# Kernel optimization log

Hardware: AMD Instinct MI355X
Metric: run time of the kernel (lower is better)

## Reference

```python
import jax, jax.numpy as jnp
import numpy as np

BN_EPS = 1e-5


def setup_inputs() -> dict:
    key = jax.random.key(0)
    ks = jax.random.split(key, 5)
    B, C, T, V = 64, 64, 300, 25
    O, N = 128, 8  # out_channels, num_adj
    x = jax.random.normal(ks[0], (B, C, T, V), dtype=jnp.float32)
    # adjacency: row-normalized so powers A^1..A^8 stay well-conditioned
    A = jax.random.uniform(ks[1], (V, V), dtype=jnp.float32)
    A = A / jnp.sum(A, axis=1, keepdims=True)
    W = jax.random.normal(ks[2], (N, O // N, C), dtype=jnp.float32) * 0.05  # per-branch 1x1 conv weights
    Wr = jax.random.normal(ks[3], (O, C), dtype=jnp.float32) * 0.05          # residual 1x1 conv weight
    br = jnp.zeros((O,), dtype=jnp.float32)                                   # residual conv bias
    gamma = jnp.ones((O,), dtype=jnp.float32)
    beta = jnp.zeros((O,), dtype=jnp.float32)
    return {"x": x, "A": A, "W": W, "Wr": Wr, "br": br, "gamma": gamma, "beta": beta}


def reference(x, A, W, Wr, br, gamma, beta):
    # x: [B, C, T, V]; A: [V, V]; W: [num_adj, O//num_adj, C]
    num_adj = W.shape[0]
    outs = []
    A_pow = A  # A_list[i] = A^(i+1), matching _split_adjacency_matrix
    for i in range(num_adj):
        g = jnp.einsum('bcfj,jk->bcfk', x, A_pow)           # graph conv on joints
        outs.append(jnp.einsum('oc,bcfk->bofk', W[i], g))   # 1x1 conv (no bias)
        A_pow = A_pow @ A
    out = jnp.concatenate(outs, axis=1)                      # [B, O, T, V]
    residual = jnp.einsum('oc,bcfj->bofj', Wr, x) + br[None, :, None, None]
    out = out + residual
    # BatchNorm2d (training-mode batch statistics over B, T, V per channel)
    mean = jnp.mean(out, axis=(0, 2, 3), keepdims=True)
    var = jnp.var(out, axis=(0, 2, 3), keepdims=True)
    out = gamma[None, :, None, None] * (out - mean) / jnp.sqrt(var + BN_EPS) + beta[None, :, None, None]
    return jax.nn.relu(out)
```

## Files before the change

### kernel.cpp

```cpp
#include <hip/hip_runtime.h>
#include <hip/hip_bf16.h>

#define B_  64
#define C_  64
#define T_  300
#define V_  25
#define O_  128
#define TV  (T_*V_)
#define BTV (B_*T_*V_)
#define HS_STRIDE 258
#define HS_ROWS 57
#define NPF 9600

typedef __bf16 bf16x8 __attribute__((ext_vector_type(8)));
typedef float f32x4 __attribute__((ext_vector_type(4)));

#define WSB_AF    0ull
#define WSB_WT    18432ull
#define WSB_PSC   51200ull
#define WSB_PSQ   4966400ull
#define WSB_SCL   9881600ull
#define WSB_SFT   9882112ull
#define WSB_Y     9882624ull
#define WS_NEED2  132762624ull

static __device__ __forceinline__ unsigned short f2bf(float f) {
    unsigned int u = __float_as_uint(f);
    unsigned int r = (u + 0x7fffu + ((u >> 16) & 1u)) >> 16;
    return (unsigned short)r;
}
static __device__ __forceinline__ float bf2f(unsigned short u) {
    return __uint_as_float(((unsigned int)u) << 16);
}

__global__ __launch_bounds__(256) void k_prep(const float* __restrict__ A,
                                              const float* __restrict__ W,
                                              const float* __restrict__ Wr,
                                              unsigned short* __restrict__ AF,
                                              unsigned short* __restrict__ Wt) {
    const int tid = threadIdx.x;
    if (blockIdx.x == 0) {
        __shared__ float Pall[8][625];
        for (int p = tid; p < 625; p += 256) Pall[0][p] = A[p];
        __syncthreads();
        for (int i = 1; i < 8; i++) {
            for (int p = tid; p < 625; p += 256) {
                int r = p / 25, c = p - r * 25;
                float s = 0.f;
                #pragma unroll 5
                for (int j = 0; j < 25; j++) s = fmaf(Pall[i-1][r*25 + j], A[j*25 + c], s);
                Pall[i][p] = s;
            }
            __syncthreads();
        }
        for (int idx = tid; idx < 18 * 64; idx += 256) {
            int fi = idx >> 6, l = idx & 63, qq = l >> 4, tt = l & 15;
            unsigned short v[8];
            #pragma unroll
            for (int e = 0; e < 8; e++) {
                int j = qq * 8 + e;
                float val = 0.f;
                if (fi < 16) {
                    int i = fi >> 1, k = (fi & 1) * 16 + tt;
                    if (j < 25 && k < 25) val = Pall[i][j * 25 + k];
                } else {
                    int k = (fi - 16) * 16 + tt;
                    if (j < 25 && k < 25 && j == k) val = 1.f;
                }
                v[e] = f2bf(val);
            }
            *(uint4*)(AF + idx * 8) = *(uint4*)v;
        }
    } else {
        const int oc = tid;
        const float* src = (oc < 128) ? (W + oc * 64) : (Wr + (oc - 128) * 64);
        unsigned short row[64];
        #pragma unroll
        for (int c = 0; c < 64; c++) row[c] = f2bf(src[c]);
        #pragma unroll
        for (int cc = 0; cc < 8; cc++)
            *(uint4*)(Wt + oc * 64 + cc * 8) = *(uint4*)(row + cc * 8);
    }
}

__global__ __launch_bounds__(256, 4) void k_fuse(const float* __restrict__ x,
                                                 const unsigned short* __restrict__ Wt,
                                                 const unsigned short* __restrict__ AF,
                                                 unsigned short* __restrict__ Yg,
                                                 float* __restrict__ psc,
                                                 float* __restrict__ psq) {
    __shared__ __align__(16) unsigned short SM[4096 + HS_ROWS * HS_STRIDE];
    unsigned short* As = SM;
    unsigned short* Hs = SM + 4096;
    const int tg = blockIdx.x, b = blockIdx.y;
    const int tid = threadIdx.x, wv = tid >> 6, ln = tid & 63;
    const int q = ln >> 4, t = ln & 15;

    for (int p = tid; p < 1600; p += 256) {
        int c = p / 25, e = p - c * 25;
        float2 f = *(const float2*)(x + ((size_t)(b * 64 + c)) * TV + tg * 50 + e * 2);
        int r0 = e * 2;
        As[r0 * 64 + (((c >> 3) ^ (r0 & 7)) << 3) + (c & 7)]         = f2bf(f.x);
        As[(r0+1) * 64 + (((c >> 3) ^ ((r0+1) & 7)) << 3) + (c & 7)] = f2bf(f.y);
    }
    for (int w = tid; w < 448; w += 256) ((unsigned int*)As)[1600 + w] = 0u;
    for (int w = tid; w < 903; w += 256) ((unsigned int*)Hs)[6450 + w] = 0u;
    __syncthreads();

    {
        const int oq = wv;
        f32x4 acc[4][4] = {};
        #pragma unroll
        for (int ks = 0; ks < 2; ks++) {
            const unsigned short* wb = Wt + (oq * 64 + t) * 64 + q * 8 + ks * 32;
            bf16x8 bv[4], af[4];
            #pragma unroll
            for (int ni = 0; ni < 4; ni++) bv[ni] = *(const bf16x8*)(wb + ni * 1024);
            #pragma unroll
            for (int mi = 0; mi < 4; mi++) {
                int row = mi * 16 + t;
                af[mi] = *(const bf16x8*)(As + row * 64 + (((ks * 4 + q) ^ (row & 7)) << 3));
            }
            #pragma unroll
            for (int mi = 0; mi < 4; mi++)
                #pragma unroll
                for (int ni = 0; ni < 4; ni++)
                    acc[mi][ni] = __builtin_amdgcn_mfma_f32_16x16x32_bf16(bv[ni], af[mi], acc[mi][ni], 0, 0, 0);
        }
        #pragma unroll
        for (int mi = 0; mi < 4; mi++) {
            int row = mi * 16 + t;
            if (row < 50) {
                #pragma unroll
                for (int ni = 0; ni < 4; ni++) {
                    int co = oq * 64 + ni * 16 + q * 4;
                    unsigned int* dst = (unsigned int*)(Hs + row * HS_STRIDE + co);
                    dst[0] = (unsigned int)f2bf(acc[mi][ni][0]) | ((unsigned int)f2bf(acc[mi][ni][1]) << 16);
                    dst[1] = (unsigned int)f2bf(acc[mi][ni][2]) | ((unsigned int)f2bf(acc[mi][ni][3]) << 16);
                }
            }
        }
    }
    __syncthreads();

    const int s = wv >> 1, bh = wv & 1;
    const bf16x8* AFp = (const bf16x8*)AF;
    const bf16x8 id0 = AFp[16 * 64 + ln];
    const bf16x8 id1 = AFp[17 * 64 + ln];
    f32x4 acc2[4][2];
    #pragma unroll
    for (int ii = 0; ii < 4; ii++) { acc2[ii][0] = (f32x4){0,0,0,0}; acc2[ii][1] = (f32x4){0,0,0,0}; }
    const int rowq = (s * 25 + q * 8) * HS_STRIDE + t;
    #pragma unroll
    for (int ii = 0; ii < 4; ii++) {
        const int i = bh * 4 + ii;
        unsigned short hm[8], hr[8];
        #pragma unroll
        for (int e = 0; e < 8; e++) {
            int a = rowq + e * HS_STRIDE + i * 16;
            hm[e] = Hs[a];
            hr[e] = Hs[a + 128];
        }
        bf16x8 bm = *(bf16x8*)hm;
        bf16x8 brs = *(bf16x8*)hr;
        bf16x8 a0 = AFp[(i * 2 + 0) * 64 + ln];
        bf16x8 a1 = AFp[(i * 2 + 1) * 64 + ln];
        acc2[ii][0] = __builtin_amdgcn_mfma_f32_16x16x32_bf16(id0, brs, acc2[ii][0], 0, 0, 0);
        acc2[ii][1] = __builtin_amdgcn_mfma_f32_16x16x32_bf16(id1, brs, acc2[ii][1], 0, 0, 0);
        acc2[ii][0] = __builtin_amdgcn_mfma_f32_16x16x32_bf16(a0, bm, acc2[ii][0], 0, 0, 0);
        acc2[ii][1] = __builtin_amdgcn_mfma_f32_16x16x32_bf16(a1, bm, acc2[ii][1], 0, 0, 0);
    }
    float* ps = (float*)SM;
    float* qs = ps + 256;
    #pragma unroll
    for (int ii = 0; ii < 4; ii++) {
        float si = 0.f, qi = 0.f;
        #pragma unroll
        for (int mt = 0; mt < 2; mt++)
            #pragma unroll
            for (int r = 0; r < 4; r++) {
                float v = acc2[ii][mt][r];
                si += v; qi += v * v;
            }
        si += __shfl_xor(si, 16); si += __shfl_xor(si, 32);
        qi += __shfl_xor(qi, 16); qi += __shfl_xor(qi, 32);
        if (ln < 16) {
            ps[s * 128 + (bh * 4 + ii) * 16 + t] = si;
            qs[s * 128 + (bh * 4 + ii) * 16 + t] = qi;
        }
    }
    #pragma unroll
    for (int ii = 0; ii < 4; ii++)
        #pragma unroll
        for (int mt = 0; mt < 2; mt++)
            #pragma unroll
            for (int r = 0; r < 4; r++) {
                int k = mt * 16 + q * 4 + r;
                if (k < 25)
                    Hs[(s * 25 + k) * HS_STRIDE + (bh * 4 + ii) * 16 + t] = f2bf(acc2[ii][mt][r]);
            }
    __syncthreads();
    if (tid < 128) {
        float S = ps[tid] + ps[128 + tid];
        float Q = qs[tid] + qs[128 + tid];
        int blk = b * 150 + tg;
        psc[(size_t)blk * 128 + tid] = S;
        psq[(size_t)blk * 128 + tid] = Q;
    }
    for (int idx = tid; idx < 3200; idx += 256) {
        int o = idx / 25, w = idx - o * 25;
        unsigned int d = (unsigned int)Hs[(w * 2) * HS_STRIDE + o]
                       | ((unsigned int)Hs[(w * 2 + 1) * HS_STRIDE + o] << 16);
        *(unsigned int*)(Yg + (size_t)(b * 128 + o) * TV + tg * 50 + w * 2) = d;
    }
}

__global__ __launch_bounds__(256) void k_fin2(const float* __restrict__ psc,
                                              const float* __restrict__ psq,
                                              const float* __restrict__ gamma,
                                              const float* __restrict__ beta,
                                              float* __restrict__ scale,
                                              float* __restrict__ shift) {
    const int o = blockIdx.x, tid = threadIdx.x;
    float S = 0.f, Q = 0.f;
    for (int i = tid; i < NPF; i += 256) {
        S += psc[(size_t)i * 128 + o];
        Q += psq[(size_t)i * 128 + o];
    }
    #pragma unroll
    for (int m = 1; m < 64; m <<= 1) { S += __shfl_xor(S, m); Q += __shfl_xor(Q, m); }
    __shared__ float ls[4], lq[4];
    int w = tid >> 6;
    if ((tid & 63) == 0) { ls[w] = S; lq[w] = Q; }
    __syncthreads();
    if (tid == 0) {
        float St = ls[0] + ls[1] + ls[2] + ls[3];
        float Qt = lq[0] + lq[1] + lq[2] + lq[3];
        float inv = 1.f / (float)BTV;
        float mean = St * inv;
        float var = Qt * inv - mean * mean;
        float sc = gamma[o] / sqrtf(var + 1e-5f);
        scale[o] = sc;
        shift[o] = beta[o] - mean * sc;
    }
}

__global__ __launch_bounds__(256) void k_norm2(const unsigned short* __restrict__ Y,
                                               const float* __restrict__ scale,
                                               const float* __restrict__ shift,
                                               float* __restrict__ out) {
    size_t e0 = ((size_t)blockIdx.x * 256 + threadIdx.x) * 8;
    #pragma unroll
    for (int g = 0; g < 2; g++) {
        size_t e = e0 + (size_t)g * 4;
        int o = (int)((e / 7500) & 127);
        float sc = scale[o], sh = shift[o];
        uint2 v = *(const uint2*)(Y + e);
        float4 d;
        d.x = fmaxf(fmaf(bf2f((unsigned short)(v.x & 0xffffu)), sc, sh), 0.f);
        d.y = fmaxf(fmaf(bf2f((unsigned short)(v.x >> 16)),     sc, sh), 0.f);
        d.z = fmaxf(fmaf(bf2f((unsigned short)(v.y & 0xffffu)), sc, sh), 0.f);
        d.w = fmaxf(fmaf(bf2f((unsigned short)(v.y >> 16)),     sc, sh), 0.f);
        *(float4*)(out + e) = d;
    }
}

extern "C" void kernel_launch(void* const* d_in, const int* in_sizes, int n_in,
                              void* d_out, int out_size, void* d_ws, size_t ws_size,
                              hipStream_t stream) {
    const float* x     = (const float*)d_in[0];
    const float* A     = (const float*)d_in[1];
    const float* W     = (const float*)d_in[2];
    const float* Wr    = (const float*)d_in[3];
    const float* gamma = (const float*)d_in[5];
    const float* beta  = (const float*)d_in[6];
    float* out = (float*)d_out;
    char* wsb  = (char*)d_ws;
    if (ws_size < (size_t)WS_NEED2) return;

    unsigned short* AF  = (unsigned short*)(wsb + WSB_AF);
    unsigned short* Wt  = (unsigned short*)(wsb + WSB_WT);
    float*          psc = (float*)(wsb + WSB_PSC);
    float*          psq = (float*)(wsb + WSB_PSQ);
    float*          scl = (float*)(wsb + WSB_SCL);
    float*          sft = (float*)(wsb + WSB_SFT);
    unsigned short* Y   = (unsigned short*)(wsb + WSB_Y);

    k_prep<<<2, 256, 0, stream>>>(A, W, Wr, AF, Wt);
    k_fuse<<<dim3(150, 64), 256, 0, stream>>>(x, Wt, AF, Y, psc, psq);
    k_fin2<<<128, 256, 0, stream>>>(psc, psq, gamma, beta, scl, sft);
    k_norm2<<<30000, 256, 0, stream>>>(Y, scl, sft, out);
}
```

Before: 267.7 us.

## Double block tile to 4 time steps and transpose intermediate LDS layout with XOR swizzle

```diff
diff --git a/kernel.cpp b/kernel.cpp
--- a/kernel.cpp
+++ b/kernel.cpp
@@ -8,9 +8,7 @@
 #define O_  128
 #define TV  (T_*V_)
 #define BTV (B_*T_*V_)
-#define HS_STRIDE 258
-#define HS_ROWS 57
-#define NPF 9600
+#define NPF 4800
 
 typedef __bf16 bf16x8 __attribute__((ext_vector_type(8)));
 typedef float f32x4 __attribute__((ext_vector_type(4)));
@@ -83,32 +81,39 @@
     }
 }
 
-__global__ __launch_bounds__(256, 4) void k_fuse(const float* __restrict__ x,
+__global__ __launch_bounds__(512, 2) void k_fuse(const float* __restrict__ x,
                                                  const unsigned short* __restrict__ Wt,
                                                  const unsigned short* __restrict__ AF,
                                                  unsigned short* __restrict__ Yg,
                                                  float* __restrict__ psc,
                                                  float* __restrict__ psq) {
-    __shared__ __align__(16) unsigned short SM[4096 + HS_ROWS * HS_STRIDE];
-    unsigned short* As = SM;
-    unsigned short* Hs = SM + 4096;
+    __shared__ __align__(16) unsigned short SM[8192 + 256 * 128];
+    unsigned short* As  = SM;
+    unsigned short* Hs2 = SM + 8192;
     const int tg = blockIdx.x, b = blockIdx.y;
     const int tid = threadIdx.x, wv = tid >> 6, ln = tid & 63;
     const int q = ln >> 4, t = ln & 15;
 
-    for (int p = tid; p < 1600; p += 256) {
-        int c = p / 25, e = p - c * 25;
-        float2 f = *(const float2*)(x + ((size_t)(b * 64 + c)) * TV + tg * 50 + e * 2);
-        int r0 = e * 2;
-        As[r0 * 64 + (((c >> 3) ^ (r0 & 7)) << 3) + (c & 7)]         = f2bf(f.x);
-        As[(r0+1) * 64 + (((c >> 3) ^ ((r0+1) & 7)) << 3) + (c & 7)] = f2bf(f.y);
-    }
-    for (int w = tid; w < 448; w += 256) ((unsigned int*)As)[1600 + w] = 0u;
-    for (int w = tid; w < 903; w += 256) ((unsigned int*)Hs)[6450 + w] = 0u;
+    for (int p = tid; p < 1600; p += 512) {
+        int c = p / 25, e4 = p - c * 25;
+        float4 f = *(const float4*)(x + ((size_t)(b * 64 + c)) * TV + tg * 100 + e4 * 4);
+        float vv[4] = { f.x, f.y, f.z, f.w };
+        #pragma unroll
+        for (int u = 0; u < 4; u++) {
+            int r = e4 * 4 + u;
+            As[r * 64 + (((c >> 3) ^ (r & 7)) << 3) + (c & 7)] = f2bf(vv[u]);
+        }
+    }
+    for (int w = tid; w < 896; w += 512) ((unsigned int*)As)[3200 + w] = 0u;
+    for (int gi = tid; gi < 1024; gi += 512) {
+        int oc = gi >> 2, s = gi & 3;
+        int g = (s * 4 + 3) ^ (oc & 15);
+        *(uint4*)(Hs2 + oc * 128 + g * 8) = (uint4){0u, 0u, 0u, 0u};
+    }
     __syncthreads();
 
     {
-        const int oq = wv;
+        const int rb = wv >> 2, oq = wv & 3;
         f32x4 acc[4][4] = {};
         #pragma unroll
         for (int ks = 0; ks < 2; ks++) {
@@ -118,7 +123,7 @@
             for (int ni = 0; ni < 4; ni++) bv[ni] = *(const bf16x8*)(wb + ni * 1024);
             #pragma unroll
             for (int mi = 0; mi < 4; mi++) {
-                int row = mi * 16 + t;
+                int row = rb * 64 + mi * 16 + t;
                 af[mi] = *(const bf16x8*)(As + row * 64 + (((ks * 4 + q) ^ (row & 7)) << 3));
             }
             #pragma unroll
@@ -129,14 +134,16 @@
         }
         #pragma unroll
         for (int mi = 0; mi < 4; mi++) {
-            int row = mi * 16 + t;
-            if (row < 50) {
+            int row = rb * 64 + mi * 16 + t;
+            if (row < 100) {
+                int ss = row / 25, jj = row - ss * 25;
+                int lg = ss * 4 + (jj >> 3), off = jj & 7;
                 #pragma unroll
                 for (int ni = 0; ni < 4; ni++) {
                     int co = oq * 64 + ni * 16 + q * 4;
-                    unsigned int* dst = (unsigned int*)(Hs + row * HS_STRIDE + co);
-                    dst[0] = (unsigned int)f2bf(acc[mi][ni][0]) | ((unsigned int)f2bf(acc[mi][ni][1]) << 16);
-                    dst[1] = (unsigned int)f2bf(acc[mi][ni][2]) | ((unsigned int)f2bf(acc[mi][ni][3]) << 16);
+                    #pragma unroll
+                    for (int r = 0; r < 4; r++)
+                        Hs2[(co + r) * 128 + ((lg ^ (q * 4 + r)) << 3) + off] = f2bf(acc[mi][ni][r]);
                 }
             }
         }
@@ -150,19 +157,12 @@
     f32x4 acc2[4][2];
     #pragma unroll
     for (int ii = 0; ii < 4; ii++) { acc2[ii][0] = (f32x4){0,0,0,0}; acc2[ii][1] = (f32x4){0,0,0,0}; }
-    const int rowq = (s * 25 + q * 8) * HS_STRIDE + t;
+    const int g2 = ((s * 4 + q) ^ t) * 8;
     #pragma unroll
     for (int ii = 0; ii < 4; ii++) {
         const int i = bh * 4 + ii;
-        unsigned short hm[8], hr[8];
-        #pragma unroll
-        for (int e = 0; e < 8; e++) {
-            int a = rowq + e * HS_STRIDE + i * 16;
-            hm[e] = Hs[a];
-            hr[e] = Hs[a + 128];
-        }
-        bf16x8 bm = *(bf16x8*)hm;
-        bf16x8 brs = *(bf16x8*)hr;
+        bf16x8 bm  = *(const bf16x8*)(Hs2 + (i * 16 + t) * 128 + g2);
+        bf16x8 brs = *(const bf16x8*)(Hs2 + (128 + i * 16 + t) * 128 + g2);
         bf16x8 a0 = AFp[(i * 2 + 0) * 64 + ln];
         bf16x8 a1 = AFp[(i * 2 + 1) * 64 + ln];
         acc2[ii][0] = __builtin_amdgcn_mfma_f32_16x16x32_bf16(id0, brs, acc2[ii][0], 0, 0, 0);
@@ -171,7 +171,7 @@
         acc2[ii][1] = __builtin_amdgcn_mfma_f32_16x16x32_bf16(a1, bm, acc2[ii][1], 0, 0, 0);
     }
     float* ps = (float*)SM;
-    float* qs = ps + 256;
+    float* qs = ps + 512;
     #pragma unroll
     for (int ii = 0; ii < 4; ii++) {
         float si = 0.f, qi = 0.f;
@@ -190,28 +190,38 @@
         }
     }
     #pragma unroll
-    for (int ii = 0; ii < 4; ii++)
+    for (int ii = 0; ii < 4; ii++) {
+        const int o = (bh * 4 + ii) * 16 + t;
         #pragma unroll
         for (int mt = 0; mt < 2; mt++)
             #pragma unroll
             for (int r = 0; r < 4; r++) {
                 int k = mt * 16 + q * 4 + r;
                 if (k < 25)
-                    Hs[(s * 25 + k) * HS_STRIDE + (bh * 4 + ii) * 16 + t] = f2bf(acc2[ii][mt][r]);
-            }
+                    Hs2[o * 128 + (((s * 4 + (k >> 3)) ^ t) << 3) + (k & 7)] = f2bf(acc2[ii][mt][r]);
+            }
+    }
     __syncthreads();
     if (tid < 128) {
-        float S = ps[tid] + ps[128 + tid];
-        float Q = qs[tid] + qs[128 + tid];
-        int blk = b * 150 + tg;
+        float S = ps[tid] + ps[128 + tid] + ps[256 + tid] + ps[384 + tid];
+        float Q = qs[tid] + qs[128 + tid] + qs[256 + tid] + qs[384 + tid];
+        int blk = b * 75 + tg;
         psc[(size_t)blk * 128 + tid] = S;
         psq[(size_t)blk * 128 + tid] = Q;
     }
-    for (int idx = tid; idx < 3200; idx += 256) {
+    for (int idx = tid; idx < 3200; idx += 512) {
         int o = idx / 25, w = idx - o * 25;
-        unsigned int d = (unsigned int)Hs[(w * 2) * HS_STRIDE + o]
-                       | ((unsigned int)Hs[(w * 2 + 1) * HS_STRIDE + o] << 16);
-        *(unsigned int*)(Yg + (size_t)(b * 128 + o) * TV + tg * 50 + w * 2) = d;
+        unsigned short vv[4];
+        #pragma unroll
+        for (int e = 0; e < 4; e++) {
+            int tk = w * 4 + e;
+            int ss = tk / 25, kk = tk - ss * 25;
+            vv[e] = Hs2[o * 128 + (((ss * 4 + (kk >> 3)) ^ (o & 15)) << 3) + (kk & 7)];
+        }
+        uint2 d;
+        d.x = (unsigned int)vv[0] | ((unsigned int)vv[1] << 16);
+        d.y = (unsigned int)vv[2] | ((unsigned int)vv[3] << 16);
+        *(uint2*)(Yg + (size_t)(b * 128 + o) * TV + tg * 100 + w * 4) = d;
     }
 }
 
@@ -287,7 +297,7 @@
     unsigned short* Y   = (unsigned short*)(wsb + WSB_Y);
 
     k_prep<<<2, 256, 0, stream>>>(A, W, Wr, AF, Wt);
-    k_fuse<<<dim3(150, 64), 256, 0, stream>>>(x, Wt, AF, Y, psc, psq);
+    k_fuse<<<dim3(75, 64), 512, 0, stream>>>(x, Wt, AF, Y, psc, psq);
     k_fin2<<<128, 256, 0, stream>>>(psc, psq, gamma, beta, scl, sft);
     k_norm2<<<30000, 256, 0, stream>>>(Y, scl, sft, out);
 }
```

Measured after the change: 237.0 us. 11.5% less time.
